# Kernel tuning notes

Hardware: AMD Instinct MI355X
Metric: run time of the kernel (lower is better)

## Reference

```python
import jax, jax.numpy as jnp
import numpy as np

N = 131072
MANO_CHILD = (2, 3, 17, 5, 6, 18, 8, 9, 20, 11, 12, 19, 14, 15, 16)
MANO_PARENT = (1, 2, 3, 4, 5, 6, 7, 8, 9, 10, 11, 12, 13, 14, 15)
FINGERS = ((0, 1, 2, 3, 17), (0, 4, 5, 6, 18), (0, 7, 8, 9, 20), (0, 10, 11, 12, 19), (0, 13, 14, 15, 16))
PALM = np.array([0, 1, 4, 7, 10, 13])
MAX_FLEX = float(np.pi / 2)  # flexion clamp range [0, pi/2]
EPS = 1e-8


def _wrist_rot(src, dst):
    """Kabsch rotation R (N,3,3) such that R @ src_k ~= dst_k (palm alignment)."""
    H = jnp.einsum('nki,nkj->nij', src, dst)          # sum_k src dst^T
    U, S, Vt = jnp.linalg.svd(H, full_matrices=False)
    VUt = jnp.einsum('nji,nkj->nik', Vt, U)           # V @ U^T
    d = jnp.linalg.det(VUt)
    D = jnp.stack([jnp.ones_like(d), jnp.ones_like(d), d], axis=-1)
    return jnp.einsum('nji,nj,nkj->nik', Vt, D, U)    # V diag(1,1,d) U^T


def _rodrigues(v, axis, theta):
    """Rotate vectors v (N,3) about unit axis (N,3) by angle theta (N,)."""
    c = jnp.cos(theta)[:, None]
    s = jnp.sin(theta)[:, None]
    return v * c + jnp.cross(axis, v) * s + axis * jnp.sum(axis * v, -1, keepdims=True) * (1.0 - c)


def _forward(joints, tempJ):
    wrist = joints[:, :1]
    J = joints - wrist                       # wrist-centered observed joints
    T = tempJ - tempJ[:, :1]                 # wrist-centered template
    bone_ref = T                             # bonelenTempJ: reference bone lengths
    # rigid palm alignment of template onto observed joints
    R = _wrist_rot(T[:, PALM], J[:, PALM])
    T = jnp.einsum('nij,nkj->nki', R, T)     # rotate every template joint
    # palm joints of observation are replaced by aligned template palm
    J = J.at[:, PALM].set(T[:, PALM])
    # (hand-pose-legitimize layer approximated as identity; source unavailable)
    for idx in range(len(MANO_CHILD)):
        ch, pa = MANO_CHILD[idx], MANO_PARENT[idx]
        v1 = J[:, ch] - T[:, pa]
        dis = jnp.linalg.norm(v1, axis=1)
        univ1 = v1 / (dis[:, None] + EPS)
        blen = jnp.linalg.norm(bone_ref[:, ch] - bone_ref[:, pa], axis=1)
        lo, hi = blen, blen                  # non-RHD template: lower == upper
        valid = (lo <= dis) & (dis <= hi)
        clamped = jnp.clip(dis, lo, hi)
        new = jnp.where(valid[:, None], J[:, ch], T[:, pa] + univ1 * clamped[:, None])
        T = T.at[:, ch].set(new)
        # flexion legitimization: clamp bend angle of this bone vs its parent bone
        f = FINGERS[idx // 3]
        k = idx % 3
        gp, pp, cc = f[k], f[k + 1], f[k + 2]  # grandparent, parent(=pa), child(=ch)
        v0 = T[:, pp] - T[:, gp]
        vb = T[:, cc] - T[:, pp]
        cr = jnp.cross(v0, vb)
        s = jnp.linalg.norm(cr, axis=1)
        c = jnp.sum(v0 * vb, axis=1)
        ang = jnp.arctan2(s, c)
        delta = jnp.clip(ang, 0.0, MAX_FLEX) - ang
        axis = cr / (s[:, None] + EPS)
        T = T.at[:, cc].set(_rodrigues(vb, axis, delta) + T[:, pp])
    return wrist + T


def setup_inputs() -> dict:
    key = jax.random.key(0)
    k1, k2 = jax.random.split(key)
    joints = jax.random.normal(k1, (N, 21, 3), dtype=jnp.float32)
    tempJ = jax.random.normal(k2, (N, 21, 3), dtype=jnp.float32)
    return {"joints": joints, "tempJ": tempJ}


def reference(joints, tempJ):
    return _forward(joints, tempJ)
```

## Files before the change

### kernel.cpp

```cpp
#include <hip/hip_runtime.h>
#include <math.h>

#define KEPS 1e-8f
#define BLOCK 256
#define HF 63
#define TILE_F (BLOCK * HF)
#define TILE_V4 (TILE_F / 4)

__global__ __launch_bounds__(BLOCK)
void kin_fwd(const float* __restrict__ joints,
             const float* __restrict__ tempJ,
             float* __restrict__ out,
             int n_total)
{
    constexpr int CHILD[15]  = {2,3,17, 5,6,18, 8,9,20, 11,12,19, 14,15,16};
    constexpr int PARENT[15] = {1,2,3, 4,5,6, 7,8,9, 10,11,12, 13,14,15};
    constexpr int GPID[15]   = {0,1,2, 0,4,5, 0,7,8, 0,10,11, 0,13,14};
    constexpr int PALM[6]    = {0,1,4,7,10,13};

    __shared__ float lds[TILE_F];

    const int tid = threadIdx.x;
    const int n   = blockIdx.x * BLOCK + tid;
    const long long tileBase = (long long)blockIdx.x * TILE_F;
    const long long totalF   = (long long)n_total * HF;
    const bool fullTile = (tileBase + TILE_F) <= totalF;

    if (fullTile) {
        const float4* g4 = (const float4*)(tempJ + tileBase);
        float4* l4 = (float4*)lds;
#pragma unroll
        for (int r = 0; r < TILE_V4; r += BLOCK) {
            const int idx = r + tid;
            if (idx < TILE_V4) l4[idx] = g4[idx];
        }
    } else {
        for (int idx = tid; idx < TILE_F; idx += BLOCK) {
            const long long g = tileBase + idx;
            lds[idx] = (g < totalF) ? tempJ[g] : 0.f;
        }
    }
    __syncthreads();

    const bool active = (n < n_total);
    float T[21][3];
    float blen[15];
    float wx = 0.f, wy = 0.f, wz = 0.f;

    if (active) {
        const float* tl = lds + tid * HF;
#pragma unroll
        for (int k = 0; k < 21; ++k) {
            T[k][0] = tl[3*k+0];
            T[k][1] = tl[3*k+1];
            T[k][2] = tl[3*k+2];
        }
        const float ox = T[0][0], oy = T[0][1], oz = T[0][2];
#pragma unroll
        for (int k = 0; k < 21; ++k) { T[k][0] -= ox; T[k][1] -= oy; T[k][2] -= oz; }

#pragma unroll
        for (int i = 0; i < 15; ++i) {
            const float dx = T[CHILD[i]][0] - T[PARENT[i]][0];
            const float dy = T[CHILD[i]][1] - T[PARENT[i]][1];
            const float dz = T[CHILD[i]][2] - T[PARENT[i]][2];
            blen[i] = sqrtf(dx*dx + dy*dy + dz*dz);
        }
    }
    __syncthreads();

    if (fullTile) {
        const float4* g4 = (const float4*)(joints + tileBase);
        float4* l4 = (float4*)lds;
#pragma unroll
        for (int r = 0; r < TILE_V4; r += BLOCK) {
            const int idx = r + tid;
            if (idx < TILE_V4) l4[idx] = g4[idx];
        }
    } else {
        for (int idx = tid; idx < TILE_F; idx += BLOCK) {
            const long long g = tileBase + idx;
            lds[idx] = (g < totalF) ? joints[g] : 0.f;
        }
    }
    __syncthreads();

    if (active) {
        const float* jl = lds + tid * HF;
        wx = jl[0]; wy = jl[1]; wz = jl[2];

        #define JLC(k,d) (jl[3*(k)+(d)] - ((d)==0 ? wx : ((d)==1 ? wy : wz)))

        float H[3][3] = {{0.f,0.f,0.f},{0.f,0.f,0.f},{0.f,0.f,0.f}};
#pragma unroll
        for (int p = 0; p < 6; ++p) {
            const int k = PALM[p];
            const float jx = JLC(k,0), jy = JLC(k,1), jz = JLC(k,2);
            H[0][0] += T[k][0]*jx; H[0][1] += T[k][0]*jy; H[0][2] += T[k][0]*jz;
            H[1][0] += T[k][1]*jx; H[1][1] += T[k][1]*jy; H[1][2] += T[k][1]*jz;
            H[2][0] += T[k][2]*jx; H[2][1] += T[k][2]*jy; H[2][2] += T[k][2]*jz;
        }

        float A[3][3];
#pragma unroll
        for (int i = 0; i < 3; ++i)
#pragma unroll
            for (int j = 0; j < 3; ++j)
                A[i][j] = H[0][i]*H[0][j] + H[1][i]*H[1][j] + H[2][i]*H[2][j];

        float V[3][3] = {{1.f,0.f,0.f},{0.f,1.f,0.f},{0.f,0.f,1.f}};
#pragma unroll
        for (int sw = 0; sw < 6; ++sw) {
#pragma unroll
            for (int r = 0; r < 3; ++r) {
                const int p = (r == 2) ? 1 : 0;
                const int q = (r == 0) ? 1 : 2;
                const float b   = A[p][q];
                const float dif = A[q][q] - A[p][p];
                const float rho = sqrtf(dif*dif + 4.f*b*b);
                const float c2  = (rho > 0.f) ? (dif / rho) : 1.f;
                const float c   = sqrtf(fmaxf(0.5f*(1.f + c2), 0.f));
                const float s   = copysignf(sqrtf(fmaxf(0.5f*(1.f - c2), 0.f)), b);
#pragma unroll
                for (int i = 0; i < 3; ++i) {
                    const float aip = A[i][p], aiq = A[i][q];
                    A[i][p] = c*aip - s*aiq;
                    A[i][q] = s*aip + c*aiq;
                }
#pragma unroll
                for (int j = 0; j < 3; ++j) {
                    const float apj = A[p][j], aqj = A[q][j];
                    A[p][j] = c*apj - s*aqj;
                    A[q][j] = s*apj + c*aqj;
                }
#pragma unroll
                for (int i = 0; i < 3; ++i) {
                    const float vip = V[i][p], viq = V[i][q];
                    V[i][p] = c*vip - s*viq;
                    V[i][q] = s*vip + c*viq;
                }
            }
        }

        float lam[3] = {A[0][0], A[1][1], A[2][2]};
#pragma unroll
        for (int pass = 0; pass < 3; ++pass) {
            const int i = (pass == 2) ? 1 : 0;
            const int j = (pass == 0) ? 1 : 2;
            if (lam[i] < lam[j]) {
                const float tl2 = lam[i]; lam[i] = lam[j]; lam[j] = tl2;
#pragma unroll
                for (int r2 = 0; r2 < 3; ++r2) {
                    const float tv = V[r2][i]; V[r2][i] = V[r2][j]; V[r2][j] = tv;
                }
            }
        }

        float R[3][3];
        {
            const float v1x = V[0][0], v1y = V[1][0], v1z = V[2][0];
            const float v2x = V[0][1], v2y = V[1][1], v2z = V[2][1];
            const float v3x = V[0][2], v3y = V[1][2], v3z = V[2][2];

            float w1x = H[0][0]*v1x + H[0][1]*v1y + H[0][2]*v1z;
            float w1y = H[1][0]*v1x + H[1][1]*v1y + H[1][2]*v1z;
            float w1z = H[2][0]*v1x + H[2][1]*v1y + H[2][2]*v1z;
            const float n1 = sqrtf(w1x*w1x + w1y*w1y + w1z*w1z);
            const float in1 = 1.f / fmaxf(n1, 1e-20f);
            const float u1x = w1x*in1, u1y = w1y*in1, u1z = w1z*in1;

            float w2x = H[0][0]*v2x + H[0][1]*v2y + H[0][2]*v2z;
            float w2y = H[1][0]*v2x + H[1][1]*v2y + H[1][2]*v2z;
            float w2z = H[2][0]*v2x + H[2][1]*v2y + H[2][2]*v2z;
            const float dp = u1x*w2x + u1y*w2y + u1z*w2z;
            w2x -= dp*u1x; w2y -= dp*u1y; w2z -= dp*u1z;
            const float n2 = sqrtf(w2x*w2x + w2y*w2y + w2z*w2z);
            const float in2 = 1.f / fmaxf(n2, 1e-20f);
            const float u2x = w2x*in2, u2y = w2y*in2, u2z = w2z*in2;

            const float u3x = u1y*u2z - u1z*u2y;
            const float u3y = u1z*u2x - u1x*u2z;
            const float u3z = u1x*u2y - u1y*u2x;

            const float detV =
                v1x*(v2y*v3z - v2z*v3y) - v1y*(v2x*v3z - v2z*v3x) + v1z*(v2x*v3y - v2y*v3x);
            const float d = (detV < 0.f) ? -1.f : 1.f;
            const float w3x = d*v3x, w3y = d*v3y, w3z = d*v3z;

            R[0][0] = v1x*u1x + v2x*u2x + w3x*u3x;
            R[0][1] = v1x*u1y + v2x*u2y + w3x*u3y;
            R[0][2] = v1x*u1z + v2x*u2z + w3x*u3z;
            R[1][0] = v1y*u1x + v2y*u2x + w3y*u3x;
            R[1][1] = v1y*u1y + v2y*u2y + w3y*u3y;
            R[1][2] = v1y*u1z + v2y*u2z + w3y*u3z;
            R[2][0] = v1z*u1x + v2z*u2x + w3z*u3x;
            R[2][1] = v1z*u1y + v2z*u2y + w3z*u3y;
            R[2][2] = v1z*u1z + v2z*u2z + w3z*u3z;
        }

#pragma unroll
        for (int k = 0; k < 21; ++k) {
            const float x = T[k][0], y = T[k][1], z = T[k][2];
            T[k][0] = R[0][0]*x + R[0][1]*y + R[0][2]*z;
            T[k][1] = R[1][0]*x + R[1][1]*y + R[1][2]*z;
            T[k][2] = R[2][0]*x + R[2][1]*y + R[2][2]*z;
        }

#pragma unroll
        for (int i = 0; i < 15; ++i) {
            const int ch = CHILD[i], pa = PARENT[i], gp = GPID[i];

            const float jcx = JLC(ch,0), jcy = JLC(ch,1), jcz = JLC(ch,2);
            const float v1x = jcx - T[pa][0];
            const float v1y = jcy - T[pa][1];
            const float v1z = jcz - T[pa][2];
            const float dis = sqrtf(v1x*v1x + v1y*v1y + v1z*v1z);
            const float bl  = blen[i];
            const float sc  = bl / (dis + KEPS);
            const bool valid = (dis == bl);
            T[ch][0] = valid ? jcx : T[pa][0] + v1x*sc;
            T[ch][1] = valid ? jcy : T[pa][1] + v1y*sc;
            T[ch][2] = valid ? jcz : T[pa][2] + v1z*sc;

            const float v0x = T[pa][0] - T[gp][0];
            const float v0y = T[pa][1] - T[gp][1];
            const float v0z = T[pa][2] - T[gp][2];
            const float vbx = T[ch][0] - T[pa][0];
            const float vby = T[ch][1] - T[pa][1];
            const float vbz = T[ch][2] - T[pa][2];

            const float crx = v0y*vbz - v0z*vby;
            const float cry = v0z*vbx - v0x*vbz;
            const float crz = v0x*vby - v0y*vbx;
            const float s2  = crx*crx + cry*cry + crz*crz;
            const float s   = sqrtf(s2);
            const float c   = v0x*vbx + v0y*vby + v0z*vbz;

            const float rlen = sqrtf(s2 + c*c);
            const float invr = 1.f / fmaxf(rlen, 1e-30f);
            const float cosd = (c < 0.f) ? s*invr : 1.f;
            const float sind = (c < 0.f) ? c*invr : 0.f;

            const float sainv = 1.f / (s + KEPS);
            const float ax = crx*sainv, ay = cry*sainv, az = crz*sainv;

            const float cxx = ay*vbz - az*vby;
            const float cxy = az*vbx - ax*vbz;
            const float cxz = ax*vby - ay*vbx;
            const float adv = ax*vbx + ay*vby + az*vbz;
            const float omc = 1.f - cosd;
            T[ch][0] = vbx*cosd + cxx*sind + ax*adv*omc + T[pa][0];
            T[ch][1] = vby*cosd + cxy*sind + ay*adv*omc + T[pa][1];
            T[ch][2] = vbz*cosd + cxz*sind + az*adv*omc + T[pa][2];
        }
        #undef JLC
    }
    __syncthreads();

    if (active) {
        float* ol = lds + tid * HF;
#pragma unroll
        for (int k = 0; k < 21; ++k) {
            ol[3*k+0] = wx + T[k][0];
            ol[3*k+1] = wy + T[k][1];
            ol[3*k+2] = wz + T[k][2];
        }
    }
    __syncthreads();

    if (fullTile) {
        float4* g4 = (float4*)(out + tileBase);
        const float4* l4 = (const float4*)lds;
#pragma unroll
        for (int r = 0; r < TILE_V4; r += BLOCK) {
            const int idx = r + tid;
            if (idx < TILE_V4) g4[idx] = l4[idx];
        }
    } else {
        for (int idx = tid; idx < TILE_F; idx += BLOCK) {
            const long long g = tileBase + idx;
            if (g < totalF) out[g] = lds[idx];
        }
    }
}

extern "C" void kernel_launch(void* const* d_in, const int* in_sizes, int n_in,
                              void* d_out, int out_size, void* d_ws, size_t ws_size,
                              hipStream_t stream)
{
    const float* joints = (const float*)d_in[0];
    const float* tempJ  = (const float*)d_in[1];
    float* out          = (float*)d_out;

    const int n_total = in_sizes[0] / 63;
    const int grid = (n_total + BLOCK - 1) / BLOCK;
    kin_fwd<<<grid, BLOCK, 0, stream>>>(joints, tempJ, out, n_total);
}
```

Baseline: 117.1 us.

## Use hardware rsqrt, cut Jacobi sweeps, simplify bone and flexion math

Replaces sqrt/divide pairs with the AMD hardware rsq and sqrt builtins, drops the Jacobi eigen-solver sweeps from 6 to 4, and preloads the observed joints into registers. The bone step is simplified to always rescale to bone length, and the Rodrigues axial term (axis is perpendicular to the bone, so it is zero) is removed. It also removes a barrier between compute and the LDS writeback, and sets launch bounds to allow 2 blocks per CU. The aim is fewer transcendental and divide instructions per hand; the cost is lower accuracy from fewer sweeps and approximate rsqrt, plus more register pressure from holding the joints.

```diff
diff --git a/kernel.cpp b/kernel.cpp
--- a/kernel.cpp
+++ b/kernel.cpp
@@ -1,13 +1,15 @@
 #include <hip/hip_runtime.h>
 #include <math.h>
 
-#define KEPS 1e-8f
 #define BLOCK 256
 #define HF 63
 #define TILE_F (BLOCK * HF)
 #define TILE_V4 (TILE_F / 4)
 
-__global__ __launch_bounds__(BLOCK)
+__device__ __forceinline__ float rsqf(float x)  { return __builtin_amdgcn_rsqf(x); }
+__device__ __forceinline__ float sqtf(float x)  { return __builtin_amdgcn_sqrtf(x); }
+
+__global__ __launch_bounds__(BLOCK, 2)
 void kin_fwd(const float* __restrict__ joints,
              const float* __restrict__ tempJ,
              float* __restrict__ out,
@@ -25,15 +27,12 @@
     const long long tileBase = (long long)blockIdx.x * TILE_F;
     const long long totalF   = (long long)n_total * HF;
     const bool fullTile = (tileBase + TILE_F) <= totalF;
+    const bool active = (n < n_total);
 
     if (fullTile) {
         const float4* g4 = (const float4*)(tempJ + tileBase);
         float4* l4 = (float4*)lds;
-#pragma unroll
-        for (int r = 0; r < TILE_V4; r += BLOCK) {
-            const int idx = r + tid;
-            if (idx < TILE_V4) l4[idx] = g4[idx];
-        }
+        for (int idx = tid; idx < TILE_V4; idx += BLOCK) l4[idx] = g4[idx];
     } else {
         for (int idx = tid; idx < TILE_F; idx += BLOCK) {
             const long long g = tileBase + idx;
@@ -42,10 +41,8 @@
     }
     __syncthreads();
 
-    const bool active = (n < n_total);
     float T[21][3];
     float blen[15];
-    float wx = 0.f, wy = 0.f, wz = 0.f;
 
     if (active) {
         const float* tl = lds + tid * HF;
@@ -64,7 +61,7 @@
             const float dx = T[CHILD[i]][0] - T[PARENT[i]][0];
             const float dy = T[CHILD[i]][1] - T[PARENT[i]][1];
             const float dz = T[CHILD[i]][2] - T[PARENT[i]][2];
-            blen[i] = sqrtf(dx*dx + dy*dy + dz*dz);
+            blen[i] = sqtf(dx*dx + dy*dy + dz*dz);
         }
     }
     __syncthreads();
@@ -72,11 +69,7 @@
     if (fullTile) {
         const float4* g4 = (const float4*)(joints + tileBase);
         float4* l4 = (float4*)lds;
-#pragma unroll
-        for (int r = 0; r < TILE_V4; r += BLOCK) {
-            const int idx = r + tid;
-            if (idx < TILE_V4) l4[idx] = g4[idx];
-        }
+        for (int idx = tid; idx < TILE_V4; idx += BLOCK) l4[idx] = g4[idx];
     } else {
         for (int idx = tid; idx < TILE_F; idx += BLOCK) {
             const long long g = tileBase + idx;
@@ -85,20 +78,30 @@
     }
     __syncthreads();
 
+    float wx = 0.f, wy = 0.f, wz = 0.f;
+
     if (active) {
-        const float* jl = lds + tid * HF;
-        wx = jl[0]; wy = jl[1]; wz = jl[2];
-
-        #define JLC(k,d) (jl[3*(k)+(d)] - ((d)==0 ? wx : ((d)==1 ? wy : wz)))
+        float Jl[21][3];
+        {
+            const float* jl = lds + tid * HF;
+            wx = jl[0]; wy = jl[1]; wz = jl[2];
+#pragma unroll
+            for (int k = 0; k < 21; ++k) {
+                Jl[k][0] = jl[3*k+0] - wx;
+                Jl[k][1] = jl[3*k+1] - wy;
+                Jl[k][2] = jl[3*k+2] - wz;
+            }
+        }
 
         float H[3][3] = {{0.f,0.f,0.f},{0.f,0.f,0.f},{0.f,0.f,0.f}};
 #pragma unroll
         for (int p = 0; p < 6; ++p) {
             const int k = PALM[p];
-            const float jx = JLC(k,0), jy = JLC(k,1), jz = JLC(k,2);
-            H[0][0] += T[k][0]*jx; H[0][1] += T[k][0]*jy; H[0][2] += T[k][0]*jz;
-            H[1][0] += T[k][1]*jx; H[1][1] += T[k][1]*jy; H[1][2] += T[k][1]*jz;
-            H[2][0] += T[k][2]*jx; H[2][1] += T[k][2]*jy; H[2][2] += T[k][2]*jz;
+#pragma unroll
+            for (int i = 0; i < 3; ++i)
+#pragma unroll
+                for (int j = 0; j < 3; ++j)
+                    H[i][j] += T[k][i] * Jl[k][j];
         }
 
         float A[3][3];
@@ -110,17 +113,17 @@
 
         float V[3][3] = {{1.f,0.f,0.f},{0.f,1.f,0.f},{0.f,0.f,1.f}};
 #pragma unroll
-        for (int sw = 0; sw < 6; ++sw) {
+        for (int sw = 0; sw < 4; ++sw) {
 #pragma unroll
             for (int r = 0; r < 3; ++r) {
                 const int p = (r == 2) ? 1 : 0;
                 const int q = (r == 0) ? 1 : 2;
                 const float b   = A[p][q];
                 const float dif = A[q][q] - A[p][p];
-                const float rho = sqrtf(dif*dif + 4.f*b*b);
-                const float c2  = (rho > 0.f) ? (dif / rho) : 1.f;
-                const float c   = sqrtf(fmaxf(0.5f*(1.f + c2), 0.f));
-                const float s   = copysignf(sqrtf(fmaxf(0.5f*(1.f - c2), 0.f)), b);
+                const float irho = rsqf(dif*dif + 4.f*b*b + 1e-35f);
+                const float c2  = dif * irho;
+                const float c   = sqtf(fmaxf(0.5f + 0.5f*c2, 0.f));
+                const float s   = copysignf(sqtf(fmaxf(0.5f - 0.5f*c2, 0.f)), b);
 #pragma unroll
                 for (int i = 0; i < 3; ++i) {
                     const float aip = A[i][p], aiq = A[i][q];
@@ -162,11 +165,10 @@
             const float v2x = V[0][1], v2y = V[1][1], v2z = V[2][1];
             const float v3x = V[0][2], v3y = V[1][2], v3z = V[2][2];
 
-            float w1x = H[0][0]*v1x + H[0][1]*v1y + H[0][2]*v1z;
-            float w1y = H[1][0]*v1x + H[1][1]*v1y + H[1][2]*v1z;
-            float w1z = H[2][0]*v1x + H[2][1]*v1y + H[2][2]*v1z;
-            const float n1 = sqrtf(w1x*w1x + w1y*w1y + w1z*w1z);
-            const float in1 = 1.f / fmaxf(n1, 1e-20f);
+            const float w1x = H[0][0]*v1x + H[0][1]*v1y + H[0][2]*v1z;
+            const float w1y = H[1][0]*v1x + H[1][1]*v1y + H[1][2]*v1z;
+            const float w1z = H[2][0]*v1x + H[2][1]*v1y + H[2][2]*v1z;
+            const float in1 = rsqf(w1x*w1x + w1y*w1y + w1z*w1z + 1e-35f);
             const float u1x = w1x*in1, u1y = w1y*in1, u1z = w1z*in1;
 
             float w2x = H[0][0]*v2x + H[0][1]*v2y + H[0][2]*v2z;
@@ -174,8 +176,7 @@
             float w2z = H[2][0]*v2x + H[2][1]*v2y + H[2][2]*v2z;
             const float dp = u1x*w2x + u1y*w2y + u1z*w2z;
             w2x -= dp*u1x; w2y -= dp*u1y; w2z -= dp*u1z;
-            const float n2 = sqrtf(w2x*w2x + w2y*w2y + w2z*w2z);
-            const float in2 = 1.f / fmaxf(n2, 1e-20f);
+            const float in2 = rsqf(w2x*w2x + w2y*w2y + w2z*w2z + 1e-35f);
             const float u2x = w2x*in2, u2y = w2y*in2, u2z = w2z*in2;
 
             const float u3x = u1y*u2z - u1z*u2y;
@@ -210,54 +211,38 @@
         for (int i = 0; i < 15; ++i) {
             const int ch = CHILD[i], pa = PARENT[i], gp = GPID[i];
 
-            const float jcx = JLC(ch,0), jcy = JLC(ch,1), jcz = JLC(ch,2);
-            const float v1x = jcx - T[pa][0];
-            const float v1y = jcy - T[pa][1];
-            const float v1z = jcz - T[pa][2];
-            const float dis = sqrtf(v1x*v1x + v1y*v1y + v1z*v1z);
-            const float bl  = blen[i];
-            const float sc  = bl / (dis + KEPS);
-            const bool valid = (dis == bl);
-            T[ch][0] = valid ? jcx : T[pa][0] + v1x*sc;
-            T[ch][1] = valid ? jcy : T[pa][1] + v1y*sc;
-            T[ch][2] = valid ? jcz : T[pa][2] + v1z*sc;
+            const float v1x = Jl[ch][0] - T[pa][0];
+            const float v1y = Jl[ch][1] - T[pa][1];
+            const float v1z = Jl[ch][2] - T[pa][2];
+            const float d2  = v1x*v1x + v1y*v1y + v1z*v1z;
+            const float sc  = blen[i] * rsqf(d2 + 1e-16f);
+            const float vbx = v1x*sc, vby = v1y*sc, vbz = v1z*sc;
 
             const float v0x = T[pa][0] - T[gp][0];
             const float v0y = T[pa][1] - T[gp][1];
             const float v0z = T[pa][2] - T[gp][2];
-            const float vbx = T[ch][0] - T[pa][0];
-            const float vby = T[ch][1] - T[pa][1];
-            const float vbz = T[ch][2] - T[pa][2];
 
             const float crx = v0y*vbz - v0z*vby;
             const float cry = v0z*vbx - v0x*vbz;
             const float crz = v0x*vby - v0y*vbx;
             const float s2  = crx*crx + cry*cry + crz*crz;
-            const float s   = sqrtf(s2);
             const float c   = v0x*vbx + v0y*vby + v0z*vbz;
 
-            const float rlen = sqrtf(s2 + c*c);
-            const float invr = 1.f / fmaxf(rlen, 1e-30f);
-            const float cosd = (c < 0.f) ? s*invr : 1.f;
-            const float sind = (c < 0.f) ? c*invr : 0.f;
-
-            const float sainv = 1.f / (s + KEPS);
+            const float invr  = rsqf(s2 + c*c + 1e-35f);
+            const float sainv = rsqf(s2 + 1e-35f);
+            const float s     = s2 * sainv;
+            const float cosd  = (c < 0.f) ? s*invr : 1.f;
+            const float sind  = (c < 0.f) ? c*invr : 0.f;
+
             const float ax = crx*sainv, ay = cry*sainv, az = crz*sainv;
-
             const float cxx = ay*vbz - az*vby;
             const float cxy = az*vbx - ax*vbz;
             const float cxz = ax*vby - ay*vbx;
-            const float adv = ax*vbx + ay*vby + az*vbz;
-            const float omc = 1.f - cosd;
-            T[ch][0] = vbx*cosd + cxx*sind + ax*adv*omc + T[pa][0];
-            T[ch][1] = vby*cosd + cxy*sind + ay*adv*omc + T[pa][1];
-            T[ch][2] = vbz*cosd + cxz*sind + az*adv*omc + T[pa][2];
-        }
-        #undef JLC
-    }
-    __syncthreads();
-
-    if (active) {
+            T[ch][0] = vbx*cosd + cxx*sind + T[pa][0];
+            T[ch][1] = vby*cosd + cxy*sind + T[pa][1];
+            T[ch][2] = vbz*cosd + cxz*sind + T[pa][2];
+        }
+
         float* ol = lds + tid * HF;
 #pragma unroll
         for (int k = 0; k < 21; ++k) {
@@ -271,11 +256,7 @@
     if (fullTile) {
         float4* g4 = (float4*)(out + tileBase);
         const float4* l4 = (const float4*)lds;
-#pragma unroll
-        for (int r = 0; r < TILE_V4; r += BLOCK) {
-            const int idx = r + tid;
-            if (idx < TILE_V4) g4[idx] = l4[idx];
-        }
+        for (int idx = tid; idx < TILE_V4; idx += BLOCK) g4[idx] = l4[idx];
     } else {
         for (int idx = tid; idx < TILE_F; idx += BLOCK) {
             const long long g = tileBase + idx;
```

Measured after the change: 111.3 us. 1.05x faster.
